# Performance work log

Hardware: AMD Instinct MI355X
Metric: run time of the kernel (lower is better)

Reference implementation:

```python
import jax, jax.numpy as jnp
import numpy as np

RMIN, RMAX, MAX_PHASE = 0.9, 1.0, 6.283


def setup_inputs() -> dict:
    key = jax.random.key(0)
    ks = jax.random.split(key, 12)
    Bsz, T, U, O, S, H = 16, 4096, 128, 128, 256, 512
    inp = jax.random.normal(ks[0], (Bsz, T, U), dtype=jnp.float32)
    # stable complex diagonal: |lambda| in [RMIN, RMAX], phase in [0, MAX_PHASE]
    r = RMIN + (RMAX - RMIN) * jax.random.uniform(ks[1], (S,), dtype=jnp.float32)
    theta = MAX_PHASE * jax.random.uniform(ks[2], (S,), dtype=jnp.float32)
    Lambda_re = r * jnp.cos(theta)
    Lambda_im = r * jnp.sin(theta)
    B = jax.random.normal(ks[3], (S, U), dtype=jnp.float32) / np.sqrt(U)
    C = jax.random.normal(ks[4], (O, S), dtype=jnp.float32) / np.sqrt(S)
    D = jax.random.normal(ks[5], (O, U), dtype=jnp.float32) / np.sqrt(U)
    W1 = jax.random.normal(ks[6], (H, O), dtype=jnp.float32) / np.sqrt(O)
    W2 = jax.random.normal(ks[7], (H, H), dtype=jnp.float32) / np.sqrt(H)
    W3 = jax.random.normal(ks[8], (O, H), dtype=jnp.float32) / np.sqrt(H)
    Wlin = jax.random.normal(ks[9], (O, U), dtype=jnp.float32) / np.sqrt(U)
    return {"input": inp, "Lambda_re": Lambda_re, "Lambda_im": Lambda_im,
            "B": B, "C": C, "D": D, "W1": W1, "W2": W2, "W3": W3, "Wlin": Wlin}


def _linear_scan(lam, bu):
    # lam: (S,) complex; bu: (B, T, S) complex
    # h_t = lam * h_{t-1} + bu_t, h_0 = 0  (work-efficient associative scan)
    A = jnp.broadcast_to(lam[None, None, :], bu.shape)

    def combine(c1, c2):
        a1, x1 = c1
        a2, x2 = c2
        return a1 * a2, a2 * x1 + x2

    _, h = jax.lax.associative_scan(combine, (A, bu), axis=1)
    return h


def reference(input, Lambda_re, Lambda_im, B, C, D, W1, W2, W3, Wlin):
    lam = (Lambda_re + 1j * Lambda_im).astype(jnp.complex64)        # (S,)
    bu = jnp.einsum('btu,su->bts', input, B).astype(jnp.complex64)   # (B,T,S)
    h = _linear_scan(lam, bu)                                        # (B,T,S) complex
    # LRU readout: real(C h) + D u
    y = jnp.einsum('bts,os->bto', h, C.astype(jnp.complex64)).real \
        + jnp.einsum('btu,ou->bto', input, D)                        # (B,T,O)
    # MLP: Linear->SiLU->Linear->ReLU->Linear (no biases)
    z = jax.nn.silu(y @ W1.T)
    z = jax.nn.relu(z @ W2.T)
    mlp_out = z @ W3.T                                               # (B,T,O)
    # residual linear path
    return mlp_out + input @ Wlin.T
```

## Files before the change

### kernel.cpp

```cpp
#include <hip/hip_runtime.h>
#include <hip/hip_bf16.h>

#define BSZ 16
#define TT 4096
#define UU 128
#define OO 128
#define SS 256
#define HH 512
#define BT (BSZ*TT)
#define CLEN 64
#define NCH (TT/CLEN)

using bf16x8 = __attribute__((ext_vector_type(8))) short;
using f32x4  = __attribute__((ext_vector_type(4))) float;

__device__ __forceinline__ unsigned short f2bf(float x){
  union { float f; unsigned int u; } v; v.f = x;
  unsigned int r = v.u + 0x7fffu + ((v.u >> 16) & 1u);
  return (unsigned short)(r >> 16);
}
__device__ __forceinline__ float bf2f(unsigned short h){
  union { float f; unsigned int u; } v; v.u = ((unsigned int)h) << 16;
  return v.f;
}

#define GLD16(g, s) __builtin_amdgcn_global_load_lds( \
    (const __attribute__((address_space(1))) unsigned int*)(g), \
    (__attribute__((address_space(3))) unsigned int*)(s), 16, 0, 0)

__global__ __launch_bounds__(256) void split_k(const float* __restrict__ x,
                                               unsigned short* __restrict__ H,
                                               unsigned short* __restrict__ L, int n4){
  int i = blockIdx.x * 256 + threadIdx.x;
  if (i >= n4) return;
  float4 v = ((const float4*)x)[i];
  unsigned short h0 = f2bf(v.x), h1 = f2bf(v.y), h2 = f2bf(v.z), h3 = f2bf(v.w);
  ushort4 hh = make_ushort4(h0, h1, h2, h3);
  ushort4 ll = make_ushort4(f2bf(v.x - bf2f(h0)), f2bf(v.y - bf2f(h1)),
                            f2bf(v.z - bf2f(h2)), f2bf(v.w - bf2f(h3)));
  ((ushort4*)H)[i] = hh;
  ((ushort4*)L)[i] = ll;
}

struct WJobs {
  const float* src[7];
  unsigned short* H[7];
  unsigned short* L[7];
  int end4[7];
};
__global__ __launch_bounds__(256) void split_w(WJobs j, int total4){
  int i = blockIdx.x * 256 + threadIdx.x;
  if (i >= total4) return;
  int t = 0, base = 0;
  #pragma unroll
  for (int k = 0; k < 7; k++){
    if (i >= j.end4[k]){ t = k + 1; base = j.end4[k]; }
  }
  int idx = i - base;
  float4 v = ((const float4*)j.src[t])[idx];
  unsigned short h0 = f2bf(v.x), h1 = f2bf(v.y), h2 = f2bf(v.z), h3 = f2bf(v.w);
  ushort4 hh = make_ushort4(h0, h1, h2, h3);
  ushort4 ll = make_ushort4(f2bf(v.x - bf2f(h0)), f2bf(v.y - bf2f(h1)),
                            f2bf(v.z - bf2f(h2)), f2bf(v.w - bf2f(h3)));
  ((ushort4*)j.H[t])[idx] = hh;
  ((ushort4*)j.L[t])[idx] = ll;
}

__global__ __launch_bounds__(256, 2) void gemm_split(
    const unsigned short* __restrict__ AH1, const unsigned short* __restrict__ AL1,
    const unsigned short* __restrict__ BH1, const unsigned short* __restrict__ BL1, int K1, int f1,
    const unsigned short* __restrict__ AH2, const unsigned short* __restrict__ AL2,
    const unsigned short* __restrict__ BH2, const unsigned short* __restrict__ BL2, int K2, int f2,
    unsigned short* __restrict__ outH, unsigned short* __restrict__ outL,
    float* __restrict__ outF, int Nout, int EPI,
    const float* __restrict__ lre, const float* __restrict__ lim,
    float2* __restrict__ ends)
{
  __shared__ __align__(16) unsigned short SM[32768];
  unsigned short* Ah = SM;
  unsigned short* Al = SM + 8192;
  unsigned short* Bh = SM + 16384;
  unsigned short* Bl = SM + 24576;

  const int tid = threadIdx.x;
  const int mb = blockIdx.x, nb = blockIdx.y;
  const int l = tid & 63, w = tid >> 6;
  const int wr = w >> 1, wc = w & 1;
  const int fr = l & 15, fq = l >> 4;

  f32x4 acc[4][4];
  #pragma unroll
  for (int m = 0; m < 4; m++)
    #pragma unroll
    for (int n = 0; n < 4; n++) acc[m][n] = f32x4{0.f, 0.f, 0.f, 0.f};

  const int nkt = (K1 + K2) >> 5;

  auto STAGE = [&](int buf, int kt){
    const int k0 = kt << 5;
    const unsigned short *aH, *aL, *bH, *bL; int st, kk, flg;
    if (k0 < K1){ aH = AH1; aL = AL1; bH = BH1; bL = BL1; st = K1; kk = k0; flg = f1; }
    else        { aH = AH2; aL = AL2; bH = BH2; bL = BL2; st = K2; kk = k0 - K1; flg = f2; }
    #pragma unroll
    for (int it = 0; it < 2; it++){
      int seg = tid + it * 256;
      int r = seg >> 2, c4 = seg & 3;
      int sc = (c4 ^ ((r >> 1) & 3)) << 3;
      size_t go = (size_t)(mb*128 + r) * st + kk + sc;
      size_t gb = (size_t)(nb*128 + r) * st + kk + sc;
      int lo = buf*4096 + r*32 + c4*8;
      GLD16(aH + go, Ah + lo);
      if (flg & 1) GLD16(aL + go, Al + lo);
      GLD16(bH + gb, Bh + lo);
      if (flg & 2) GLD16(bL + gb, Bl + lo);
    }
  };

  STAGE(0, 0);
  __syncthreads();

  for (int kt = 0; kt < nkt; kt++){
    const int cur = kt & 1;
    const int flg = ((kt << 5) < K1) ? f1 : f2;
    if (kt + 1 < nkt) STAGE(cur ^ 1, kt + 1);

    bf16x8 a_h[4], a_l[4], b_h[4], b_l[4];
    #pragma unroll
    for (int m = 0; m < 4; m++){
      int lra = wr*64 + m*16 + fr;
      int ra = cur*4096 + lra*32 + ((fq ^ ((lra >> 1) & 3)) << 3);
      a_h[m] = *(const bf16x8*)&Ah[ra];
      if (flg & 1) a_l[m] = *(const bf16x8*)&Al[ra];
      int lrb = wc*64 + m*16 + fr;
      int rb = cur*4096 + lrb*32 + ((fq ^ ((lrb >> 1) & 3)) << 3);
      b_h[m] = *(const bf16x8*)&Bh[rb];
      if (flg & 2) b_l[m] = *(const bf16x8*)&Bl[rb];
    }
    __builtin_amdgcn_s_setprio(1);
    #pragma unroll
    for (int m = 0; m < 4; m++)
      #pragma unroll
      for (int n = 0; n < 4; n++)
        acc[m][n] = __builtin_amdgcn_mfma_f32_16x16x32_bf16(a_h[m], b_h[n], acc[m][n], 0, 0, 0);
    if (flg & 1)
      #pragma unroll
      for (int m = 0; m < 4; m++)
        #pragma unroll
        for (int n = 0; n < 4; n++)
          acc[m][n] = __builtin_amdgcn_mfma_f32_16x16x32_bf16(a_l[m], b_h[n], acc[m][n], 0, 0, 0);
    if (flg & 2)
      #pragma unroll
      for (int m = 0; m < 4; m++)
        #pragma unroll
        for (int n = 0; n < 4; n++)
          acc[m][n] = __builtin_amdgcn_mfma_f32_16x16x32_bf16(a_h[m], b_l[n], acc[m][n], 0, 0, 0);
    __builtin_amdgcn_s_setprio(0);

    __syncthreads();
  }

  float* fl = (float*)SM;
  #pragma unroll
  for (int m = 0; m < 4; m++)
    #pragma unroll
    for (int n = 0; n < 4; n++)
      #pragma unroll
      for (int j = 0; j < 4; j++)
        fl[(wr*64 + m*16 + fq*4 + j)*128 + wc*64 + n*16 + fr] = acc[m][n][j];
  __syncthreads();
  #pragma unroll
  for (int it = 0; it < 8; it++){
    int task = tid + (it << 8);
    int rl = task >> 4, cg = task & 15;
    float4 v0 = *(const float4*)&fl[rl*128 + cg*8];
    float4 v1 = *(const float4*)&fl[rl*128 + cg*8 + 4];
    size_t o = (size_t)(mb*128 + rl) * Nout + nb*128 + cg*8;
    if (EPI == 0){
      *(float4*)(outF + o)     = v0;
      *(float4*)(outF + o + 4) = v1;
    } else {
      float xv[8] = {v0.x,v0.y,v0.z,v0.w,v1.x,v1.y,v1.z,v1.w};
      union { unsigned short us[8]; uint4 v; } ph, pl;
      #pragma unroll
      for (int e = 0; e < 8; e++){
        float x = xv[e];
        if (EPI == 2)      x = x / (1.f + __expf(-x));
        else if (EPI == 3) x = fmaxf(x, 0.f);
        ph.us[e] = f2bf(x);
        pl.us[e] = f2bf(x - bf2f(ph.us[e]));
      }
      *(uint4*)(outH + o) = ph.v;
      if (outL) *(uint4*)(outL + o) = pl.v;
    }
  }
  if (ends){
    int c = tid >> 7, sl = tid & 127;
    int b = mb >> 5, chunk = ((mb & 31) << 1) + c;
    int s = nb*128 + sl;
    float lr = lre[s], li = lim[s];
    float hr = 0.f, hi2 = 0.f;
    for (int t = 0; t < 64; t++){
      float x = fl[(c*64 + t)*128 + sl];
      float nr = fmaf(lr, hr, fmaf(-li, hi2, x));
      float ni = fmaf(lr, hi2, li * hr);
      hr = nr; hi2 = ni;
    }
    ends[((size_t)(b*NCH + chunk))*SS + s] = make_float2(hr, hi2);
  }
}

__global__ __launch_bounds__(256, 4) void gemm_h(
    const unsigned short* __restrict__ A, const unsigned short* __restrict__ B, int K,
    unsigned short* __restrict__ outH, float* __restrict__ outF, int Nout, int EPI)
{
  __shared__ __align__(16) unsigned short SM[16384];
  unsigned short* Ah = SM;
  unsigned short* Bh = SM + 8192;

  const int tid = threadIdx.x;
  const int mb = blockIdx.x, nb = blockIdx.y;
  const int l = tid & 63, w = tid >> 6;
  const int wr = w >> 1, wc = w & 1;
  const int fr = l & 15, fq = l >> 4;

  f32x4 acc[4][4];
  #pragma unroll
  for (int m = 0; m < 4; m++)
    #pragma unroll
    for (int n = 0; n < 4; n++) acc[m][n] = f32x4{0.f, 0.f, 0.f, 0.f};

  const int nkt = K >> 5;

  auto STAGE = [&](int buf, int kt){
    const int kk = kt << 5;
    #pragma unroll
    for (int it = 0; it < 2; it++){
      int seg = tid + it * 256;
      int r = seg >> 2, c4 = seg & 3;
      int sc = (c4 ^ ((r >> 1) & 3)) << 3;
      int lo = buf*4096 + r*32 + c4*8;
      GLD16(A + (size_t)(mb*128 + r) * K + kk + sc, Ah + lo);
      GLD16(B + (size_t)(nb*128 + r) * K + kk + sc, Bh + lo);
    }
  };

  STAGE(0, 0);
  __syncthreads();

  for (int kt = 0; kt < nkt; kt++){
    const int cur = kt & 1;
    if (kt + 1 < nkt) STAGE(cur ^ 1, kt + 1);

    bf16x8 a_h[4], b_h[4];
    #pragma unroll
    for (int m = 0; m < 4; m++){
      int lra = wr*64 + m*16 + fr;
      a_h[m] = *(const bf16x8*)&Ah[cur*4096 + lra*32 + ((fq ^ ((lra >> 1) & 3)) << 3)];
      int lrb = wc*64 + m*16 + fr;
      b_h[m] = *(const bf16x8*)&Bh[cur*4096 + lrb*32 + ((fq ^ ((lrb >> 1) & 3)) << 3)];
    }
    __builtin_amdgcn_s_setprio(1);
    #pragma unroll
    for (int m = 0; m < 4; m++)
      #pragma unroll
      for (int n = 0; n < 4; n++)
        acc[m][n] = __builtin_amdgcn_mfma_f32_16x16x32_bf16(a_h[m], b_h[n], acc[m][n], 0, 0, 0);
    __builtin_amdgcn_s_setprio(0);

    __syncthreads();
  }

  float* fl = (float*)SM;
  #pragma unroll
  for (int h = 0; h < 2; h++){
    if (wr == h){
      #pragma unroll
      for (int m = 0; m < 4; m++)
        #pragma unroll
        for (int n = 0; n < 4; n++)
          #pragma unroll
          for (int j = 0; j < 4; j++)
            fl[(m*16 + fq*4 + j)*128 + wc*64 + n*16 + fr] = acc[m][n][j];
    }
    __syncthreads();
    #pragma unroll
    for (int it = 0; it < 4; it++){
      int task = tid + (it << 8);
      int rl = task >> 4, cg = task & 15;
      float4 v0 = *(const float4*)&fl[rl*128 + cg*8];
      float4 v1 = *(const float4*)&fl[rl*128 + cg*8 + 4];
      size_t o = (size_t)(mb*128 + h*64 + rl) * Nout + nb*128 + cg*8;
      if (EPI == 0){
        *(float4*)(outF + o)     = v0;
        *(float4*)(outF + o + 4) = v1;
      } else {
        float xv[8] = {v0.x,v0.y,v0.z,v0.w,v1.x,v1.y,v1.z,v1.w};
        union { unsigned short us[8]; uint4 v; } ph;
        #pragma unroll
        for (int e = 0; e < 8; e++){
          float x = xv[e];
          if (EPI == 2)      x = x / (1.f + __expf(-x));
          else if (EPI == 3) x = fmaxf(x, 0.f);
          ph.us[e] = f2bf(x);
        }
        *(uint4*)(outH + o) = ph.v;
      }
    }
    __syncthreads();
  }
}

__global__ __launch_bounds__(256) void scan_carries(const float2* __restrict__ ends,
                                                    const float* __restrict__ lre,
                                                    const float* __restrict__ lim,
                                                    float2* __restrict__ carryin){
  const int idx = blockIdx.x * 256 + threadIdx.x;
  const int b = idx >> 8;
  const int s = idx & 255;
  float pr = lre[s], pi = lim[s];
  #pragma unroll
  for (int q = 0; q < 6; q++){
    float nr = pr*pr - pi*pi;
    float ni = 2.f * pr * pi;
    pr = nr; pi = ni;
  }
  float hr = 0.f, hi = 0.f;
  for (int c = 0; c < NCH; c++){
    size_t o = ((size_t)b*NCH + c)*SS + s;
    carryin[o] = make_float2(hr, hi);
    float2 e = ends[o];
    float nr = fmaf(pr, hr, fmaf(-pi, hi, e.x));
    float ni = fmaf(pr, hi, fmaf(pi, hr, e.y));
    hr = nr; hi = ni;
  }
}

__global__ __launch_bounds__(256) void scan_apply_v(
    const unsigned short* __restrict__ buH, const unsigned short* __restrict__ buL,
    const float* __restrict__ lre, const float* __restrict__ lim,
    const float2* __restrict__ carryin, unsigned short* __restrict__ RehH){
  const int tid = threadIdx.x;
  const int grp = tid >> 6, ln = tid & 63;
  const int chunk = blockIdx.x * 4 + grp;
  const int b = chunk >> 6, ch = chunk & 63;
  const int s0 = ln * 4;
  float lr[4], li[4], hr[4], hi[4];
  #pragma unroll
  for (int e = 0; e < 4; e++){ lr[e] = lre[s0+e]; li[e] = lim[s0+e]; }
  const float2* ci = &carryin[((size_t)(b*NCH + ch))*SS + s0];
  #pragma unroll
  for (int e = 0; e < 4; e++){ hr[e] = ci[e].x; hi[e] = ci[e].y; }
  const size_t rbase = ((size_t)b*TT + (size_t)ch*CLEN)*SS + s0;
  for (int t = 0; t < CLEN; t++){
    uint2 hv = *(const uint2*)(buH + rbase + (size_t)t*SS);
    uint2 lv = *(const uint2*)(buL + rbase + (size_t)t*SS);
    const unsigned short* hs = (const unsigned short*)&hv;
    const unsigned short* ls = (const unsigned short*)&lv;
    uint2 ov; unsigned short* os = (unsigned short*)&ov;
    #pragma unroll
    for (int e = 0; e < 4; e++){
      float x = bf2f(hs[e]) + bf2f(ls[e]);
      float nr = fmaf(lr[e], hr[e], fmaf(-li[e], hi[e], x));
      float ni = fmaf(lr[e], hi[e], li[e] * hr[e]);
      hr[e] = nr; hi[e] = ni;
      os[e] = f2bf(nr);
    }
    *(uint2*)(RehH + rbase + (size_t)t*SS) = ov;
  }
}

extern "C" void kernel_launch(void* const* d_in, const int* in_sizes, int n_in,
                              void* d_out, int out_size, void* d_ws, size_t ws_size,
                              hipStream_t stream){
  const float* inp = (const float*)d_in[0];
  const float* lre = (const float*)d_in[1];
  const float* lim = (const float*)d_in[2];
  const float* Bm  = (const float*)d_in[3];
  const float* Cm  = (const float*)d_in[4];
  const float* Dm  = (const float*)d_in[5];
  const float* W1  = (const float*)d_in[6];
  const float* W2  = (const float*)d_in[7];
  const float* W3  = (const float*)d_in[8];
  const float* Wl  = (const float*)d_in[9];
  float* out = (float*)d_out;

  char* ws = (char*)d_ws;
  size_t off = 0;
  auto alloc = [&](size_t bytes)->char*{
    char* p = ws + off; off += (bytes + 255) & ~(size_t)255; return p;
  };
  unsigned short* inH  = (unsigned short*)alloc((size_t)BT*UU*2);
  unsigned short* inL  = (unsigned short*)alloc((size_t)BT*UU*2);
  char* Rbu = alloc((size_t)BT*SS*2*2);
  unsigned short* buH = (unsigned short*)Rbu;
  unsigned short* buL = (unsigned short*)(Rbu + (size_t)BT*SS*2);
  unsigned short* z1H = (unsigned short*)Rbu;
  char* R2 = alloc((size_t)BT*HH*2);
  unsigned short* RehH = (unsigned short*)R2;
  unsigned short* yH   = (unsigned short*)(R2 + (size_t)BT*SS*2);
  unsigned short* z2H  = (unsigned short*)R2;
  unsigned short* BwH = (unsigned short*)alloc((size_t)SS*UU*2);
  unsigned short* BwL = (unsigned short*)alloc((size_t)SS*UU*2);
  unsigned short* CH_ = (unsigned short*)alloc((size_t)OO*SS*2);
  unsigned short* CL_ = (unsigned short*)alloc((size_t)OO*SS*2);
  unsigned short* DH_ = (unsigned short*)alloc((size_t)OO*UU*2);
  unsigned short* DL_ = (unsigned short*)alloc((size_t)OO*UU*2);
  unsigned short* W1H = (unsigned short*)alloc((size_t)HH*OO*2);
  unsigned short* W1L = (unsigned short*)alloc((size_t)HH*OO*2);
  unsigned short* W2H = (unsigned short*)alloc((size_t)HH*HH*2);
  unsigned short* W2L = (unsigned short*)alloc((size_t)HH*HH*2);
  unsigned short* W3H = (unsigned short*)alloc((size_t)OO*HH*2);
  unsigned short* W3L = (unsigned short*)alloc((size_t)OO*HH*2);
  unsigned short* WlH = (unsigned short*)alloc((size_t)OO*UU*2);
  unsigned short* WlL = (unsigned short*)alloc((size_t)OO*UU*2);
  float2* ends    = (float2*)alloc((size_t)BSZ*NCH*SS*8);
  float2* carryin = (float2*)alloc((size_t)BSZ*NCH*SS*8);
  if (off > ws_size) return;

  split_k<<<(BT*UU/4 + 255)/256, 256, 0, stream>>>(inp, inH, inL, BT*UU/4);
  {
    WJobs j;
    const float* srcs[7] = {Bm, Cm, Dm, W1, W2, W3, Wl};
    unsigned short* Hs[7] = {BwH, CH_, DH_, W1H, W2H, W3H, WlH};
    unsigned short* Ls[7] = {BwL, CL_, DL_, W1L, W2L, W3L, WlL};
    int n4s[7] = {SS*UU/4, OO*SS/4, OO*UU/4, HH*OO/4, HH*HH/4, OO*HH/4, OO*UU/4};
    int cum = 0;
    for (int k = 0; k < 7; k++){
      j.src[k] = srcs[k]; j.H[k] = Hs[k]; j.L[k] = Ls[k];
      cum += n4s[k]; j.end4[k] = cum;
    }
    split_w<<<(cum + 255)/256, 256, 0, stream>>>(j, cum);
  }

  gemm_split<<<dim3(BT/128, SS/128), 256, 0, stream>>>(
      inH, inL, BwH, BwL, UU, 3,
      inH, inL, BwH, BwL, 0,  3,
      buH, buL, nullptr, SS, 1,
      lre, lim, ends);

  scan_carries<<<(BSZ*SS)/256, 256, 0, stream>>>(ends, lre, lim, carryin);

  scan_apply_v<<<BSZ*NCH/4, 256, 0, stream>>>(buH, buL, lre, lim, carryin, RehH);

  gemm_split<<<dim3(BT/128, OO/128), 256, 0, stream>>>(
      RehH, RehH, CH_, CL_, SS, 2,
      inH,  inL,  DH_, DL_, UU, 3,
      yH, nullptr, nullptr, OO, 1,
      nullptr, nullptr, nullptr);

  gemm_h<<<dim3(BT/128, HH/128), 256, 0, stream>>>(
      yH, W1H, OO, z1H, nullptr, HH, 2);

  gemm_h<<<dim3(BT/128, HH/128), 256, 0, stream>>>(
      z1H, W2H, HH, z2H, nullptr, HH, 3);

  gemm_split<<<dim3(BT/128, OO/128), 256, 0, stream>>>(
      z2H, z2H, W3H, W3L, HH, 2,
      inH, inL, WlH, WlL, UU, 3,
      nullptr, nullptr, out, OO, 0,
      nullptr, nullptr, nullptr);
}
```

Baseline: 220.0 us.

## Replace LDS-staged MLP GEMM with per-wave register-direct 64x64 tiles

The two MLP GEMMs (W1 with SiLU, W2 with ReLU) no longer stage A/B tiles through double-buffered LDS. Each wave now loads its own 64x64 tile's operands straight from global memory into registers and feeds the MFMAs, and the activation plus bf16 conversion happens before one LDS-transposed coalesced store. The aim is to drop LDS traffic and per-iteration barriers. The cost is lost operand reuse across waves, since each wave refetches its A rows and B columns, which leans on L2/L1 bandwidth. The row loads are also only 16B per lane and strided by K.

```diff
diff --git a/kernel.cpp b/kernel.cpp
--- a/kernel.cpp
+++ b/kernel.cpp
@@ -209,19 +209,21 @@
   }
 }
 
-__global__ __launch_bounds__(256, 4) void gemm_h(
+__global__ __launch_bounds__(256, 3) void gemm_reg(
     const unsigned short* __restrict__ A, const unsigned short* __restrict__ B, int K,
-    unsigned short* __restrict__ outH, float* __restrict__ outF, int Nout, int EPI)
+    unsigned short* __restrict__ outH, int Nout, int EPI)
 {
-  __shared__ __align__(16) unsigned short SM[16384];
-  unsigned short* Ah = SM;
-  unsigned short* Bh = SM + 8192;
-
+  __shared__ __align__(16) unsigned short EP[64*256];
   const int tid = threadIdx.x;
-  const int mb = blockIdx.x, nb = blockIdx.y;
   const int l = tid & 63, w = tid >> 6;
-  const int wr = w >> 1, wc = w & 1;
   const int fr = l & 15, fq = l >> 4;
+  const int nW = Nout >> 6;
+  const int wid0 = blockIdx.x * 4;
+  const int wid = wid0 + w;
+  const int nb = wid & (nW - 1);
+  const int mb = wid / nW;
+  const int mb0 = wid0 / nW;
+  const int nb0 = wid0 & (nW - 1);
 
   f32x4 acc[4][4];
   #pragma unroll
@@ -229,84 +231,43 @@
     #pragma unroll
     for (int n = 0; n < 4; n++) acc[m][n] = f32x4{0.f, 0.f, 0.f, 0.f};
 
-  const int nkt = K >> 5;
-
-  auto STAGE = [&](int buf, int kt){
-    const int kk = kt << 5;
-    #pragma unroll
-    for (int it = 0; it < 2; it++){
-      int seg = tid + it * 256;
-      int r = seg >> 2, c4 = seg & 3;
-      int sc = (c4 ^ ((r >> 1) & 3)) << 3;
-      int lo = buf*4096 + r*32 + c4*8;
-      GLD16(A + (size_t)(mb*128 + r) * K + kk + sc, Ah + lo);
-      GLD16(B + (size_t)(nb*128 + r) * K + kk + sc, Bh + lo);
-    }
-  };
-
-  STAGE(0, 0);
+  const unsigned short* Ab = A + (size_t)(mb*64) * K;
+  const unsigned short* Bb = B + (size_t)(nb*64) * K;
+
+  #pragma unroll 2
+  for (int k0 = 0; k0 < K; k0 += 32){
+    bf16x8 a[4], b[4];
+    #pragma unroll
+    for (int m = 0; m < 4; m++)
+      a[m] = *(const bf16x8*)&Ab[(m*16 + fr)*K + k0 + fq*8];
+    #pragma unroll
+    for (int n = 0; n < 4; n++)
+      b[n] = *(const bf16x8*)&Bb[(n*16 + fr)*K + k0 + fq*8];
+    #pragma unroll
+    for (int m = 0; m < 4; m++)
+      #pragma unroll
+      for (int n = 0; n < 4; n++)
+        acc[m][n] = __builtin_amdgcn_mfma_f32_16x16x32_bf16(a[m], b[n], acc[m][n], 0, 0, 0);
+  }
+
+  #pragma unroll
+  for (int m = 0; m < 4; m++)
+    #pragma unroll
+    for (int n = 0; n < 4; n++)
+      #pragma unroll
+      for (int j = 0; j < 4; j++){
+        float x = acc[m][n][j];
+        if (EPI == 2)      x = x / (1.f + __expf(-x));
+        else if (EPI == 3) x = fmaxf(x, 0.f);
+        EP[(m*16 + fq*4 + j)*256 + w*64 + n*16 + fr] = f2bf(x);
+      }
   __syncthreads();
-
-  for (int kt = 0; kt < nkt; kt++){
-    const int cur = kt & 1;
-    if (kt + 1 < nkt) STAGE(cur ^ 1, kt + 1);
-
-    bf16x8 a_h[4], b_h[4];
-    #pragma unroll
-    for (int m = 0; m < 4; m++){
-      int lra = wr*64 + m*16 + fr;
-      a_h[m] = *(const bf16x8*)&Ah[cur*4096 + lra*32 + ((fq ^ ((lra >> 1) & 3)) << 3)];
-      int lrb = wc*64 + m*16 + fr;
-      b_h[m] = *(const bf16x8*)&Bh[cur*4096 + lrb*32 + ((fq ^ ((lrb >> 1) & 3)) << 3)];
-    }
-    __builtin_amdgcn_s_setprio(1);
-    #pragma unroll
-    for (int m = 0; m < 4; m++)
-      #pragma unroll
-      for (int n = 0; n < 4; n++)
-        acc[m][n] = __builtin_amdgcn_mfma_f32_16x16x32_bf16(a_h[m], b_h[n], acc[m][n], 0, 0, 0);
-    __builtin_amdgcn_s_setprio(0);
-
-    __syncthreads();
-  }
-
-  float* fl = (float*)SM;
-  #pragma unroll
-  for (int h = 0; h < 2; h++){
-    if (wr == h){
-      #pragma unroll
-      for (int m = 0; m < 4; m++)
-        #pragma unroll
-        for (int n = 0; n < 4; n++)
-          #pragma unroll
-          for (int j = 0; j < 4; j++)
-            fl[(m*16 + fq*4 + j)*128 + wc*64 + n*16 + fr] = acc[m][n][j];
-    }
-    __syncthreads();
-    #pragma unroll
-    for (int it = 0; it < 4; it++){
-      int task = tid + (it << 8);
-      int rl = task >> 4, cg = task & 15;
-      float4 v0 = *(const float4*)&fl[rl*128 + cg*8];
-      float4 v1 = *(const float4*)&fl[rl*128 + cg*8 + 4];
-      size_t o = (size_t)(mb*128 + h*64 + rl) * Nout + nb*128 + cg*8;
-      if (EPI == 0){
-        *(float4*)(outF + o)     = v0;
-        *(float4*)(outF + o + 4) = v1;
-      } else {
-        float xv[8] = {v0.x,v0.y,v0.z,v0.w,v1.x,v1.y,v1.z,v1.w};
-        union { unsigned short us[8]; uint4 v; } ph;
-        #pragma unroll
-        for (int e = 0; e < 8; e++){
-          float x = xv[e];
-          if (EPI == 2)      x = x / (1.f + __expf(-x));
-          else if (EPI == 3) x = fmaxf(x, 0.f);
-          ph.us[e] = f2bf(x);
-        }
-        *(uint4*)(outH + o) = ph.v;
-      }
-    }
-    __syncthreads();
+  #pragma unroll
+  for (int it = 0; it < 8; it++){
+    int seg = tid + (it << 8);
+    int r = seg >> 5, c8 = seg & 31;
+    *(uint4*)(outH + (size_t)(mb0*64 + r) * Nout + nb0*64 + c8*8) =
+        *(const uint4*)&EP[r*256 + c8*8];
   }
 }
 
@@ -448,11 +409,9 @@
       yH, nullptr, nullptr, OO, 1,
       nullptr, nullptr, nullptr);
 
-  gemm_h<<<dim3(BT/128, HH/128), 256, 0, stream>>>(
-      yH, W1H, OO, z1H, nullptr, HH, 2);
-
-  gemm_h<<<dim3(BT/128, HH/128), 256, 0, stream>>>(
-      z1H, W2H, HH, z2H, nullptr, HH, 3);
+  gemm_reg<<<(BT/64)*(HH/64)/4, 256, 0, stream>>>(yH, W1H, OO, z1H, HH, 2);
+
+  gemm_reg<<<(BT/64)*(HH/64)/4, 256, 0, stream>>>(z1H, W2H, HH, z2H, HH, 3);
 
   gemm_split<<<dim3(BT/128, OO/128), 256, 0, stream>>>(
       z2H, z2H, W3H, W3L, HH, 2,
```

Measured after the change: 296.8 us. 34.9% more time.
